# Kernel tuning notes

Measured on AMD Instinct MI355X. Metric: run time of the kernel, lower is better.

Reference implementation:

```python
import jax, jax.numpy as jnp
import numpy as np

EMBED_DIM = 1024
SEQ_LEN = 2048
BATCH = 4


def setup_inputs() -> dict:
    key = jax.random.key(0)
    kx, kq, kk, kv = jax.random.split(key, 4)
    scale = 1.0 / np.sqrt(EMBED_DIM)
    x = jax.random.normal(kx, (BATCH, SEQ_LEN, EMBED_DIM), dtype=jnp.float32)
    # nn.Linear weights are [out, in]; stored transposed-application here
    W_query = jax.random.normal(kq, (EMBED_DIM, EMBED_DIM), dtype=jnp.float32) * scale
    W_key = jax.random.normal(kk, (EMBED_DIM, EMBED_DIM), dtype=jnp.float32) * scale
    W_value = jax.random.normal(kv, (EMBED_DIM, EMBED_DIM), dtype=jnp.float32) * scale
    return {"x": x, "W_query": W_query, "W_key": W_key, "W_value": W_value}


def reference(x, W_query, W_key, W_value):
    # x: [B, S, D]; W_*: [D_out, D_in] (torch nn.Linear layout -> y = x @ W.T)
    B, S, D = x.shape
    q = jnp.einsum("bsd,ed->bse", x, W_query)
    k = jnp.einsum("bsd,ed->bse", x, W_key)
    v = jnp.einsum("bsd,ed->bse", x, W_value)
    scores = jnp.einsum("bqd,bkd->bqk", q, k)  # [B, S, S]
    causal = jnp.triu(jnp.ones((S, S), dtype=bool), k=1)  # True above diagonal
    scores = jnp.where(causal, -jnp.inf, scores)
    weights = jax.nn.softmax(scores / jnp.sqrt(jnp.asarray(D, x.dtype)), axis=-1)
    return jnp.einsum("bqk,bkd->bqd", weights, v)
```

## Files before the change

### kernel.cpp

```cpp
#include <hip/hip_runtime.h>
#include <stdint.h>

typedef __bf16 bf16_t;
typedef __bf16 bf16x4 __attribute__((ext_vector_type(4)));
typedef __bf16 bf16x8 __attribute__((ext_vector_type(8)));
typedef float  f32x4  __attribute__((ext_vector_type(4)));

#define AS1 __attribute__((address_space(1)))
#define AS3 __attribute__((address_space(3)))

__device__ __forceinline__ void gld_lds16(const bf16_t* g, void* s) {
  __builtin_amdgcn_global_load_lds((const AS1 uint32_t*)g, (AS3 uint32_t*)s, 16, 0, 0);
}

__global__ __launch_bounds__(256) void convert_all_kernel(
    const float* __restrict__ X,  const float* __restrict__ Wq,
    const float* __restrict__ Wk, const float* __restrict__ Wv,
    bf16_t* __restrict__ Xc, bf16_t* __restrict__ Wqc,
    bf16_t* __restrict__ Wkc, bf16_t* __restrict__ Wvc) {
  const int blk = blockIdx.x;
  const float* src; bf16_t* dst; int base;
  if (blk < 4096)      { src = X;  dst = Xc;  base = 0;    }
  else if (blk < 4608) { src = Wq; dst = Wqc; base = 4096; }
  else if (blk < 5120) { src = Wk; dst = Wkc; base = 4608; }
  else                 { src = Wv; dst = Wvc; base = 5120; }
  const int i = ((blk - base) * 256 + threadIdx.x) * 8;
  const float4 a = ((const float4*)(src + i))[0];
  const float4 b = ((const float4*)(src + i))[1];
  bf16x8 v;
  v[0] = (bf16_t)a.x; v[1] = (bf16_t)a.y; v[2] = (bf16_t)a.z; v[3] = (bf16_t)a.w;
  v[4] = (bf16_t)b.x; v[5] = (bf16_t)b.y; v[6] = (bf16_t)b.z; v[7] = (bf16_t)b.w;
  *(bf16x8*)(dst + i) = v;
}

__device__ __forceinline__ void gemm_bt_core(
    const bf16_t* __restrict__ A, int lda,
    const bf16_t* __restrict__ B, int ldb,
    int m0, int n0, int kBeg, int kEnd,
    bf16_t* As, bf16_t* Bs, f32x4 acc[4][4])
{
  const int lane = threadIdx.x & 63;
  const int wave = threadIdx.x >> 6;
  const int wm = (wave >> 1) * 64;
  const int wn = (wave & 1) * 64;
  const int fr = lane & 15;
  const int ck = lane >> 4;

  const int off0 = wave * 2048 + lane * 16;
  const int row0 = wave * 32 + (lane >> 2);
  const int row1 = row0 + 16;
  const int kg   = ((lane & 3) ^ ((row0 >> 1) & 3)) * 8;

  const bf16_t* Ar0 = A + (size_t)(m0 + row0) * lda + kg;
  const bf16_t* Ar1 = A + (size_t)(m0 + row1) * lda + kg;
  const bf16_t* Br0 = B + (size_t)(n0 + row0) * ldb + kg;
  const bf16_t* Br1 = B + (size_t)(n0 + row1) * ldb + kg;

  int aoff[4], boff[4];
#pragma unroll
  for (int i = 0; i < 4; ++i) {
    const int ra = wm + i * 16 + fr;
    const int rb = wn + i * 16 + fr;
    aoff[i] = ra * 64 + ((ck ^ ((ra >> 1) & 3)) * 16);
    boff[i] = rb * 64 + ((ck ^ ((rb >> 1) & 3)) * 16);
  }

  gld_lds16(Ar0 + kBeg, (char*)As + off0);
  gld_lds16(Ar1 + kBeg, (char*)As + off0 + 1024);
  gld_lds16(Br0 + kBeg, (char*)Bs + off0);
  gld_lds16(Br1 + kBeg, (char*)Bs + off0 + 1024);

  int cur = 0;
  for (int kt = kBeg; kt < kEnd; kt += 32) {
    const int nxt = cur ^ 1;
    if (kt + 32 < kEnd) {
      gld_lds16(Ar0 + kt + 32, (char*)As + nxt * 8192 + off0);
      gld_lds16(Ar1 + kt + 32, (char*)As + nxt * 8192 + off0 + 1024);
      gld_lds16(Br0 + kt + 32, (char*)Bs + nxt * 8192 + off0);
      gld_lds16(Br1 + kt + 32, (char*)Bs + nxt * 8192 + off0 + 1024);
      asm volatile("s_waitcnt vmcnt(4)" ::: "memory");
    } else {
      asm volatile("s_waitcnt vmcnt(0)" ::: "memory");
    }
    __builtin_amdgcn_sched_barrier(0);
    __builtin_amdgcn_s_barrier();
    __builtin_amdgcn_sched_barrier(0);

    bf16x8 af[4], bfv[4];
#pragma unroll
    for (int mi = 0; mi < 4; ++mi)
      af[mi] = *(const bf16x8*)((char*)As + cur * 8192 + aoff[mi]);
#pragma unroll
    for (int ni = 0; ni < 4; ++ni)
      bfv[ni] = *(const bf16x8*)((char*)Bs + cur * 8192 + boff[ni]);
    __builtin_amdgcn_s_setprio(1);
#pragma unroll
    for (int mi = 0; mi < 4; ++mi)
#pragma unroll
      for (int ni = 0; ni < 4; ++ni)
        acc[mi][ni] = __builtin_amdgcn_mfma_f32_16x16x32_bf16(
            af[mi], bfv[ni], acc[mi][ni], 0, 0, 0);
    __builtin_amdgcn_s_setprio(0);

    asm volatile("s_waitcnt lgkmcnt(0)" ::: "memory");
    __builtin_amdgcn_sched_barrier(0);
    __builtin_amdgcn_s_barrier();
    __builtin_amdgcn_sched_barrier(0);
    cur = nxt;
  }
}

__global__ __launch_bounds__(256) void qkv_kernel(
    const bf16_t* __restrict__ X,
    const bf16_t* __restrict__ Wq, const bf16_t* __restrict__ Wk,
    const bf16_t* __restrict__ Wv,
    bf16_t* __restrict__ Q, bf16_t* __restrict__ K, bf16_t* __restrict__ Vt)
{
  __shared__ bf16_t smem[4 * 128 * 32];
  bf16_t* As = smem;
  bf16_t* Bs = smem + 2 * 128 * 32;
  const int m0 = blockIdx.x * 128;
  const int n0 = blockIdx.y * 128;
  const int z  = blockIdx.z;
  const bf16_t* W = (z == 0) ? Wq : (z == 1) ? Wk : Wv;

  f32x4 acc[4][4] = {};
  gemm_bt_core(X, 1024, W, 1024, m0, n0, 0, 1024, As, Bs, acc);

  const int lane = threadIdx.x & 63;
  const int wave = threadIdx.x >> 6;
  const int wm = (wave >> 1) * 64, wn = (wave & 1) * 64;

  if (z < 2) {
    bf16_t* Out = z ? K : Q;
#pragma unroll
    for (int mi = 0; mi < 4; ++mi)
#pragma unroll
      for (int r = 0; r < 4; ++r) {
        const int row = m0 + wm + mi * 16 + (lane >> 4) * 4 + r;
#pragma unroll
        for (int ni = 0; ni < 4; ++ni) {
          const int col = n0 + wn + ni * 16 + (lane & 15);
          Out[(size_t)row * 1024 + col] = (bf16_t)acc[mi][ni][r];
        }
      }
  } else {
    const int b  = m0 >> 11;
    const int s0 = m0 & 2047;
    bf16_t* Vtb = Vt + (size_t)b * 1024 * 2048;
    bf16_t (*t)[136] = (bf16_t(*)[136])smem;
#pragma unroll
    for (int h = 0; h < 2; ++h) {
      __syncthreads();
      if ((wave & 1) == h) {
#pragma unroll
        for (int mi = 0; mi < 4; ++mi)
#pragma unroll
          for (int ni = 0; ni < 4; ++ni) {
            const int c   = ni * 16 + (lane & 15);
            const int row = wm + mi * 16 + (lane >> 4) * 4;
            bf16x4 v;
            v[0] = (bf16_t)acc[mi][ni][0]; v[1] = (bf16_t)acc[mi][ni][1];
            v[2] = (bf16_t)acc[mi][ni][2]; v[3] = (bf16_t)acc[mi][ni][3];
            *(bf16x4*)&t[c][row] = v;
          }
      }
      __syncthreads();
#pragma unroll
      for (int i = 0; i < 4; ++i) {
        const int u  = threadIdx.x + 256 * i;
        const int d  = u >> 4;
        const int ch = u & 15;
        bf16x8 vv = *(const bf16x8*)&t[d][ch * 8];
        *(bf16x8*)(Vtb + (size_t)(n0 + h * 64 + d) * 2048 + s0 + ch * 8) = vv;
      }
    }
  }
}

__global__ __launch_bounds__(256) void scores_exp_kernel(
    const bf16_t* __restrict__ Q, const bf16_t* __restrict__ K,
    bf16_t* __restrict__ P, float* __restrict__ partials)
{
  const int kt = blockIdx.x;
  const int mt = blockIdx.y;
  if (kt > mt) return;
  const int m0 = mt * 128;
  const int n0 = kt * 128;
  __shared__ bf16_t smem[4 * 128 * 32];
  __shared__ float rowsum[2][128];
  bf16_t* As = smem;
  bf16_t* Bs = smem + 2 * 128 * 32;
  const int batch = blockIdx.z;
  const bf16_t* Qb = Q + (size_t)batch * 2048 * 1024;
  const bf16_t* Kb = K + (size_t)batch * 2048 * 1024;
  bf16_t* Pb = P + (size_t)batch * 2048 * 2048;
  float* lp  = partials + ((size_t)batch * 16 + kt) * 2048;

  f32x4 acc[4][4] = {};
  gemm_bt_core(Qb, 1024, Kb, 1024, m0, n0, 0, 1024, As, Bs, acc);

  const int lane = threadIdx.x & 63;
  const int wave = threadIdx.x >> 6;
  const int wm = (wave >> 1) * 64, wn = (wave & 1) * 64;
  const float c = 0.04508422f;
#pragma unroll
  for (int mi = 0; mi < 4; ++mi)
#pragma unroll
    for (int r = 0; r < 4; ++r) {
      const int lrow = wm + mi * 16 + (lane >> 4) * 4 + r;
      const int row  = m0 + lrow;
      float rs = 0.f;
#pragma unroll
      for (int ni = 0; ni < 4; ++ni) {
        const int col = n0 + wn + ni * 16 + (lane & 15);
        float p = exp2f(acc[mi][ni][r] * c);
        if (col > row) p = 0.f;
        const bf16_t pb = (bf16_t)p;
        Pb[(size_t)row * 2048 + col] = pb;
        rs += (float)pb;
      }
      rs += __shfl_xor(rs, 1);
      rs += __shfl_xor(rs, 2);
      rs += __shfl_xor(rs, 4);
      rs += __shfl_xor(rs, 8);
      if ((lane & 15) == 0) rowsum[wave & 1][lrow] = rs;
    }
  __syncthreads();
  if (threadIdx.x < 128)
    lp[m0 + threadIdx.x] = rowsum[0][threadIdx.x] + rowsum[1][threadIdx.x];
}

__global__ __launch_bounds__(256) void lsum_kernel(
    const float* __restrict__ partials, float* __restrict__ Linv)
{
  const int id  = blockIdx.x * 256 + threadIdx.x;
  const int z   = id >> 11;
  const int row = id & 2047;
  const float* lp = partials + (size_t)z * 16 * 2048;
  const int tmax = row >> 7;
  float l = 0.f;
  for (int kt = 0; kt <= tmax; ++kt) l += lp[kt * 2048 + row];
  Linv[id] = 1.f / l;
}

__global__ __launch_bounds__(256) void pv_kernel(
    const bf16_t* __restrict__ P, const bf16_t* __restrict__ Vt,
    const float* __restrict__ Linv, float* __restrict__ out)
{
  __shared__ bf16_t smem[4 * 128 * 32];
  bf16_t* As = smem;
  bf16_t* Bs = smem + 2 * 128 * 32;
  const int zb = blockIdx.z;
  const int mt = ((zb >> 1) & 1) ? (15 - blockIdx.y) : blockIdx.y;
  const int m0 = mt * 128;
  const int n0 = blockIdx.x * 128;
  const bf16_t* Pb  = P  + (size_t)zb * 2048 * 2048;
  const bf16_t* Vtb = Vt + (size_t)zb * 1024 * 2048;
  const float* li = Linv + (size_t)zb * 2048;
  float* ob = out + (size_t)zb * 2048 * 1024;

  f32x4 acc[4][4] = {};
  gemm_bt_core(Pb, 2048, Vtb, 2048, m0, n0, 0, m0 + 128, As, Bs, acc);

  const int lane = threadIdx.x & 63;
  const int wave = threadIdx.x >> 6;
  const int wm = (wave >> 1) * 64, wn = (wave & 1) * 64;
#pragma unroll
  for (int mi = 0; mi < 4; ++mi)
#pragma unroll
    for (int r = 0; r < 4; ++r) {
      const int row = m0 + wm + mi * 16 + (lane >> 4) * 4 + r;
      const float inv = li[row];
#pragma unroll
      for (int ni = 0; ni < 4; ++ni) {
        const int col = n0 + wn + ni * 16 + (lane & 15);
        ob[(size_t)row * 1024 + col] = acc[mi][ni][r] * inv;
      }
    }
}

extern "C" void kernel_launch(void* const* d_in, const int* in_sizes, int n_in,
                              void* d_out, int out_size, void* d_ws, size_t ws_size,
                              hipStream_t stream) {
  const float* X  = (const float*)d_in[0];
  const float* Wq = (const float*)d_in[1];
  const float* Wk = (const float*)d_in[2];
  const float* Wv = (const float*)d_in[3];
  float* out = (float*)d_out;
  char* ws = (char*)d_ws;

  const size_t MB = 1024 * 1024;
  bf16_t* Q    = (bf16_t*)(ws + 0 * MB);
  bf16_t* K    = (bf16_t*)(ws + 16 * MB);
  bf16_t* Vt   = (bf16_t*)(ws + 32 * MB);
  bf16_t* Xc   = (bf16_t*)(ws + 48 * MB);
  bf16_t* Wqc  = (bf16_t*)(ws + 64 * MB);
  bf16_t* Wkc  = (bf16_t*)(ws + 66 * MB);
  bf16_t* Wvc  = (bf16_t*)(ws + 68 * MB);
  bf16_t* P    = (bf16_t*)(ws + 48 * MB);
  float*  Lp   = (float*)(ws + 80 * MB);
  float*  Linv = (float*)(ws + 80 * MB + 512 * 1024);

  convert_all_kernel<<<dim3(5632), 256, 0, stream>>>(X, Wq, Wk, Wv, Xc, Wqc, Wkc, Wvc);
  qkv_kernel<<<dim3(64, 8, 3), 256, 0, stream>>>(Xc, Wqc, Wkc, Wvc, Q, K, Vt);
  scores_exp_kernel<<<dim3(16, 16, 4), 256, 0, stream>>>(Q, K, P, Lp);
  lsum_kernel<<<dim3(32), 256, 0, stream>>>(Lp, Linv);
  pv_kernel<<<dim3(8, 16, 4), 256, 0, stream>>>(P, Vt, Linv, out);
}
```

Measured before the change: 241.2 us.

## Use 256x256 tiles with 512-thread blocks for QKV and score GEMMs

Adds a new GEMM core that computes a 256x256 output tile per 512-thread block. It uses a 64-wide K step, XOR-swizzled LDS double buffering of 128 KB, and 8x4 MFMA accumulators per wave. The QKV projection and scores kernels switch to this core, and their epilogues are adjusted for the larger tile, including writing two 128-column row-sum partials per block. The aim is more operand reuse per global load and fewer blocks. The cost is far fewer blocks: 384 for QKV and 144 active for scores. With one block per CU because of the LDS size, that can leave CUs idle or unbalanced.

```diff
diff --git a/kernel.cpp b/kernel.cpp
--- a/kernel.cpp
+++ b/kernel.cpp
@@ -33,6 +33,96 @@
   *(bf16x8*)(dst + i) = v;
 }
 
+__device__ __forceinline__ void gemm256_core(
+    const bf16_t* __restrict__ A, int lda,
+    const bf16_t* __restrict__ B, int ldb,
+    int m0, int n0, int kEnd,
+    char* lds, f32x4 acc[8][4])
+{
+  const int tid  = threadIdx.x;
+  const int lane = tid & 63;
+  const int wave = tid >> 6;
+  const int wm = (wave >> 2) * 128;
+  const int wn = (wave & 3) * 64;
+  const int fr = lane & 15;
+  const int ck = lane >> 4;
+
+  const int srow = tid >> 3;
+  const int sch  = tid & 7;
+  const int kgs  = (sch ^ (srow & 7)) * 8;
+  const int sdst = srow * 128 + sch * 16;
+
+  const bf16_t* Ar = A + (size_t)(m0 + srow) * lda + kgs;
+  const bf16_t* Br = B + (size_t)(n0 + srow) * ldb + kgs;
+
+  int aoffs[8], boffs[4];
+#pragma unroll
+  for (int mi = 0; mi < 8; ++mi) {
+    const int ra = wm + mi * 16 + fr;
+    aoffs[mi] = ra * 128 + ((ck ^ (ra & 7)) * 16);
+  }
+#pragma unroll
+  for (int ni = 0; ni < 4; ++ni) {
+    const int rb = wn + ni * 16 + fr;
+    boffs[ni] = rb * 128 + ((ck ^ (rb & 7)) * 16);
+  }
+
+#pragma unroll
+  for (int j = 0; j < 4; ++j) {
+    gld_lds16(Ar + (size_t)(j * 64) * lda, lds + j * 8192 + sdst);
+    gld_lds16(Br + (size_t)(j * 64) * ldb, lds + 65536 + j * 8192 + sdst);
+  }
+
+  const int NK = kEnd >> 6;
+  int cur = 0;
+  for (int t = 0; t < NK; ++t) {
+    const int nxt = cur ^ 1;
+    if (t + 1 < NK) {
+      const bf16_t* An = Ar + (t + 1) * 64;
+      const bf16_t* Bn = Br + (t + 1) * 64;
+#pragma unroll
+      for (int j = 0; j < 4; ++j) {
+        gld_lds16(An + (size_t)(j * 64) * lda, lds + nxt * 32768 + j * 8192 + sdst);
+        gld_lds16(Bn + (size_t)(j * 64) * ldb, lds + 65536 + nxt * 32768 + j * 8192 + sdst);
+      }
+      asm volatile("s_waitcnt vmcnt(8)" ::: "memory");
+    } else {
+      asm volatile("s_waitcnt vmcnt(0)" ::: "memory");
+    }
+    __builtin_amdgcn_sched_barrier(0);
+    __builtin_amdgcn_s_barrier();
+    __builtin_amdgcn_sched_barrier(0);
+
+    const char* Ab = lds + cur * 32768;
+    const char* Bb = lds + 65536 + cur * 32768;
+#pragma unroll
+    for (int ks = 0; ks < 2; ++ks) {
+      bf16x8 af[8], bfv[4];
+#pragma unroll
+      for (int mi = 0; mi < 8; ++mi)
+        af[mi] = *(const bf16x8*)(Ab + (aoffs[mi] ^ (ks * 64)));
+#pragma unroll
+      for (int ni = 0; ni < 4; ++ni)
+        bfv[ni] = *(const bf16x8*)(Bb + (boffs[ni] ^ (ks * 64)));
+      asm volatile("s_waitcnt lgkmcnt(0)" ::: "memory");
+      __builtin_amdgcn_sched_barrier(0);
+      __builtin_amdgcn_s_setprio(1);
+#pragma unroll
+      for (int mi = 0; mi < 8; ++mi)
+#pragma unroll
+        for (int ni = 0; ni < 4; ++ni)
+          acc[mi][ni] = __builtin_amdgcn_mfma_f32_16x16x32_bf16(
+              af[mi], bfv[ni], acc[mi][ni], 0, 0, 0);
+      __builtin_amdgcn_s_setprio(0);
+    }
+    asm volatile("s_waitcnt lgkmcnt(0)" ::: "memory");
+    __builtin_amdgcn_sched_barrier(0);
+    __builtin_amdgcn_s_barrier();
+    __builtin_amdgcn_sched_barrier(0);
+    cur = nxt;
+  }
+}
+
 __device__ __forceinline__ void gemm_bt_core(
     const bf16_t* __restrict__ A, int lda,
     const bf16_t* __restrict__ B, int ldb,
@@ -110,31 +200,30 @@
   }
 }
 
-__global__ __launch_bounds__(256) void qkv_kernel(
+__global__ __launch_bounds__(512) void qkv_kernel(
     const bf16_t* __restrict__ X,
     const bf16_t* __restrict__ Wq, const bf16_t* __restrict__ Wk,
     const bf16_t* __restrict__ Wv,
     bf16_t* __restrict__ Q, bf16_t* __restrict__ K, bf16_t* __restrict__ Vt)
 {
-  __shared__ bf16_t smem[4 * 128 * 32];
-  bf16_t* As = smem;
-  bf16_t* Bs = smem + 2 * 128 * 32;
-  const int m0 = blockIdx.x * 128;
-  const int n0 = blockIdx.y * 128;
+  __shared__ bf16_t smem[65536];
+  const int m0 = blockIdx.x * 256;
+  const int n0 = blockIdx.y * 256;
   const int z  = blockIdx.z;
   const bf16_t* W = (z == 0) ? Wq : (z == 1) ? Wk : Wv;
 
-  f32x4 acc[4][4] = {};
-  gemm_bt_core(X, 1024, W, 1024, m0, n0, 0, 1024, As, Bs, acc);
-
-  const int lane = threadIdx.x & 63;
-  const int wave = threadIdx.x >> 6;
-  const int wm = (wave >> 1) * 64, wn = (wave & 1) * 64;
+  f32x4 acc[8][4] = {};
+  gemm256_core(X, 1024, W, 1024, m0, n0, 1024, (char*)smem, acc);
+
+  const int tid  = threadIdx.x;
+  const int lane = tid & 63;
+  const int wave = tid >> 6;
+  const int wm = (wave >> 2) * 128, wn = (wave & 3) * 64;
 
   if (z < 2) {
     bf16_t* Out = z ? K : Q;
 #pragma unroll
-    for (int mi = 0; mi < 4; ++mi)
+    for (int mi = 0; mi < 8; ++mi)
 #pragma unroll
       for (int r = 0; r < 4; ++r) {
         const int row = m0 + wm + mi * 16 + (lane >> 4) * 4 + r;
@@ -148,64 +237,63 @@
     const int b  = m0 >> 11;
     const int s0 = m0 & 2047;
     bf16_t* Vtb = Vt + (size_t)b * 1024 * 2048;
-    bf16_t (*t)[136] = (bf16_t(*)[136])smem;
-#pragma unroll
-    for (int h = 0; h < 2; ++h) {
+    bf16_t (*tb)[264] = (bf16_t(*)[264])smem;
+#pragma unroll
+    for (int h = 0; h < 4; ++h) {
       __syncthreads();
-      if ((wave & 1) == h) {
-#pragma unroll
-        for (int mi = 0; mi < 4; ++mi)
+      if ((wave & 3) == h) {
+#pragma unroll
+        for (int mi = 0; mi < 8; ++mi)
 #pragma unroll
           for (int ni = 0; ni < 4; ++ni) {
-            const int c   = ni * 16 + (lane & 15);
-            const int row = wm + mi * 16 + (lane >> 4) * 4;
+            const int c    = ni * 16 + (lane & 15);
+            const int rowl = wm + mi * 16 + (lane >> 4) * 4;
             bf16x4 v;
             v[0] = (bf16_t)acc[mi][ni][0]; v[1] = (bf16_t)acc[mi][ni][1];
             v[2] = (bf16_t)acc[mi][ni][2]; v[3] = (bf16_t)acc[mi][ni][3];
-            *(bf16x4*)&t[c][row] = v;
+            *(bf16x4*)&tb[c][rowl] = v;
           }
       }
       __syncthreads();
 #pragma unroll
       for (int i = 0; i < 4; ++i) {
-        const int u  = threadIdx.x + 256 * i;
-        const int d  = u >> 4;
-        const int ch = u & 15;
-        bf16x8 vv = *(const bf16x8*)&t[d][ch * 8];
+        const int idx = tid + 512 * i;
+        const int d   = idx >> 5;
+        const int ch  = idx & 31;
+        bf16x8 vv = *(const bf16x8*)&tb[d][ch * 8];
         *(bf16x8*)(Vtb + (size_t)(n0 + h * 64 + d) * 2048 + s0 + ch * 8) = vv;
       }
     }
   }
 }
 
-__global__ __launch_bounds__(256) void scores_exp_kernel(
+__global__ __launch_bounds__(512) void scores_exp_kernel(
     const bf16_t* __restrict__ Q, const bf16_t* __restrict__ K,
     bf16_t* __restrict__ P, float* __restrict__ partials)
 {
   const int kt = blockIdx.x;
   const int mt = blockIdx.y;
   if (kt > mt) return;
-  const int m0 = mt * 128;
-  const int n0 = kt * 128;
-  __shared__ bf16_t smem[4 * 128 * 32];
-  __shared__ float rowsum[2][128];
-  bf16_t* As = smem;
-  bf16_t* Bs = smem + 2 * 128 * 32;
+  const int m0 = mt * 256;
+  const int n0 = kt * 256;
+  __shared__ bf16_t smem[65536];
   const int batch = blockIdx.z;
   const bf16_t* Qb = Q + (size_t)batch * 2048 * 1024;
   const bf16_t* Kb = K + (size_t)batch * 2048 * 1024;
   bf16_t* Pb = P + (size_t)batch * 2048 * 2048;
-  float* lp  = partials + ((size_t)batch * 16 + kt) * 2048;
-
-  f32x4 acc[4][4] = {};
-  gemm_bt_core(Qb, 1024, Kb, 1024, m0, n0, 0, 1024, As, Bs, acc);
-
-  const int lane = threadIdx.x & 63;
-  const int wave = threadIdx.x >> 6;
-  const int wm = (wave >> 1) * 64, wn = (wave & 1) * 64;
+  float* lp  = partials + (size_t)batch * 16 * 2048;
+
+  f32x4 acc[8][4] = {};
+  gemm256_core(Qb, 1024, Kb, 1024, m0, n0, 1024, (char*)smem, acc);
+
+  const int tid  = threadIdx.x;
+  const int lane = tid & 63;
+  const int wave = tid >> 6;
+  const int wm = (wave >> 2) * 128, wn = (wave & 3) * 64;
+  float (*rowsum)[256] = (float(*)[256])smem;
   const float c = 0.04508422f;
 #pragma unroll
-  for (int mi = 0; mi < 4; ++mi)
+  for (int mi = 0; mi < 8; ++mi)
 #pragma unroll
     for (int r = 0; r < 4; ++r) {
       const int lrow = wm + mi * 16 + (lane >> 4) * 4 + r;
@@ -224,11 +312,15 @@
       rs += __shfl_xor(rs, 2);
       rs += __shfl_xor(rs, 4);
       rs += __shfl_xor(rs, 8);
-      if ((lane & 15) == 0) rowsum[wave & 1][lrow] = rs;
+      if ((lane & 15) == 0) rowsum[wave & 3][lrow] = rs;
     }
   __syncthreads();
-  if (threadIdx.x < 128)
-    lp[m0 + threadIdx.x] = rowsum[0][threadIdx.x] + rowsum[1][threadIdx.x];
+  {
+    const int row = tid & 255;
+    const int s   = tid >> 8;
+    lp[(size_t)(2 * kt + s) * 2048 + m0 + row] =
+        rowsum[2 * s][row] + rowsum[2 * s + 1][row];
+  }
 }
 
 __global__ __launch_bounds__(256) void lsum_kernel(
@@ -303,8 +395,8 @@
   float*  Linv = (float*)(ws + 80 * MB + 512 * 1024);
 
   convert_all_kernel<<<dim3(5632), 256, 0, stream>>>(X, Wq, Wk, Wv, Xc, Wqc, Wkc, Wvc);
-  qkv_kernel<<<dim3(64, 8, 3), 256, 0, stream>>>(Xc, Wqc, Wkc, Wvc, Q, K, Vt);
-  scores_exp_kernel<<<dim3(16, 16, 4), 256, 0, stream>>>(Q, K, P, Lp);
+  qkv_kernel<<<dim3(32, 4, 3), 512, 0, stream>>>(Xc, Wqc, Wkc, Wvc, Q, K, Vt);
+  scores_exp_kernel<<<dim3(8, 8, 4), 512, 0, stream>>>(Q, K, P, Lp);
   lsum_kernel<<<dim3(32), 256, 0, stream>>>(Lp, Linv);
   pv_kernel<<<dim3(8, 16, 4), 256, 0, stream>>>(P, Vt, Linv, out);
 }
```

After: 231.9 us. 3.8% less time.
